# Performance work log

Hardware: AMD Instinct MI355X
Metric: run time of the kernel (lower is better)

## Reference

```python
import jax, jax.numpy as jnp
import numpy as np


def setup_inputs() -> dict:
    key = jax.random.key(0)
    k1, k2, k3 = jax.random.split(key, 3)
    N, D_IN, D_OUT = 8192, 512, 256
    x = jax.random.normal(k1, (N, D_IN), dtype=jnp.float32)
    # binary dense adjacency (nonzero pattern is what the torch loop uses)
    adj = jax.random.randint(k2, (N, N), 0, 2, dtype=jnp.int32)
    # weight init in torch is uniform(-stdv, stdv), stdv = 1/sqrt(out_features);
    # a normal init is fine for a numerical reference
    W = jax.random.normal(k3, (D_IN, D_OUT), dtype=jnp.float32) * (1.0 / np.sqrt(D_OUT))
    return {"x": x, "adj": adj, "W": W}


def reference(x, adj, W):
    # output = X @ W  (multiply_add(self.weight, input, None) -> mm(input, weight))
    xw = jnp.matmul(x, W)  # [N, D_OUT]
    # per-node unweighted mean over neighbors given by nonzero(adj[i])
    a = (adj != 0).astype(xw.dtype)          # [N, N] binary
    deg = jnp.sum(a, axis=1, keepdims=True)  # [N, 1] neighbor counts
    out = jnp.matmul(a, xw) / deg            # D^{-1} A (X W)
    return out
```

## Files before the change

kernel.cpp:

```cpp
#include <hip/hip_runtime.h>
#include <stdint.h>

typedef __attribute__((ext_vector_type(8))) short  bf16x8;
typedef __attribute__((ext_vector_type(4))) float  f32x4;
typedef __attribute__((ext_vector_type(4))) int    int4v;
typedef __attribute__((ext_vector_type(4))) float  float4v;
typedef __attribute__((ext_vector_type(4))) unsigned int uint4v;
typedef __attribute__((ext_vector_type(2))) unsigned int uint2v;

#define NN   8192
#define DIN  512
#define DOUT 256
#define NW   (NN / 32)

#define BM2     256
#define KSPLIT2 8
#define KS2     (NN / KSPLIT2)
#define BK2     64
#define NTK     (KS2 / BK2)

#define MFMA16(a, b, c) __builtin_amdgcn_mfma_f32_16x16x32_bf16((a), (b), (c), 0, 0, 0)

__device__ __forceinline__ unsigned short f2bf(float f) {
  unsigned u = __float_as_uint(f);
  return (unsigned short)((u + 0x7FFFu + ((u >> 16) & 1u)) >> 16);
}

__device__ __forceinline__ void gld16(const void* g, void* s) {
  __builtin_amdgcn_global_load_lds(
      (const __attribute__((address_space(1))) unsigned int*)g,
      (__attribute__((address_space(3))) unsigned int*)s, 16, 0, 0);
}

__global__ void k_wt(const float* __restrict__ W, unsigned short* __restrict__ Wt) {
  int n = blockIdx.x;
  for (int c = threadIdx.x; c < DIN; c += blockDim.x)
    Wt[n * DIN + c] = f2bf(W[c * DOUT + n]);
}

__global__ __launch_bounds__(256) void k_xwt(const float* __restrict__ x,
                                             const unsigned short* __restrict__ Wt,
                                             unsigned short* __restrict__ xw_t) {
  const int mb = blockIdx.x >> 1, nb = blockIdx.x & 1;
  const int tid = threadIdx.x;
  const int w = tid >> 6, l = tid & 63;
  const int wm = w >> 1, wn = w & 1;
  const int lr = l & 15, lg = l >> 4;
  const int m_base = mb * 128 + wm * 64;
  const int n_base = nb * 128 + wn * 64;

  f32x4 acc[4][4];
  for (int i = 0; i < 4; ++i)
    for (int j = 0; j < 4; ++j) acc[i][j] = (f32x4)0.0f;

  for (int c0 = 0; c0 < DIN; c0 += 32) {
    const int c = c0 + lg * 8;
    bf16x8 af[4], bfv[4];
#pragma unroll
    for (int mt = 0; mt < 4; ++mt) {
      const float* xp = x + (size_t)(m_base + mt * 16 + lr) * DIN + c;
      float4v x0 = *reinterpret_cast<const float4v*>(xp);
      float4v x1 = *reinterpret_cast<const float4v*>(xp + 4);
      bf16x8 a;
#pragma unroll
      for (int j = 0; j < 4; ++j) {
        a[j]     = (short)f2bf(x0[j]);
        a[4 + j] = (short)f2bf(x1[j]);
      }
      af[mt] = a;
    }
#pragma unroll
    for (int nt = 0; nt < 4; ++nt)
      bfv[nt] = *reinterpret_cast<const bf16x8*>(Wt + (size_t)(n_base + nt * 16 + lr) * DIN + c);
#pragma unroll
    for (int mt = 0; mt < 4; ++mt)
#pragma unroll
      for (int nt = 0; nt < 4; ++nt)
        acc[mt][nt] = MFMA16(af[mt], bfv[nt], acc[mt][nt]);
  }

#pragma unroll
  for (int nt = 0; nt < 4; ++nt) {
    const int n = n_base + nt * 16 + lr;
#pragma unroll
    for (int mt = 0; mt < 4; ++mt) {
      const int m = m_base + mt * 16 + lg * 4;
      unsigned short b0 = f2bf(acc[mt][nt][0]), b1 = f2bf(acc[mt][nt][1]);
      unsigned short b2 = f2bf(acc[mt][nt][2]), b3 = f2bf(acc[mt][nt][3]);
      uint2v p;
      p[0] = (unsigned)b0 | ((unsigned)b1 << 16);
      p[1] = (unsigned)b2 | ((unsigned)b3 << 16);
      *reinterpret_cast<uint2v*>(xw_t + (size_t)n * NN + m) = p;
    }
  }
}

__global__ __launch_bounds__(256) void k_pack(const int* __restrict__ adj,
                                              unsigned int* __restrict__ bits,
                                              int* __restrict__ deg) {
  __shared__ int wsum[4];
  const int tid = threadIdx.x;
  const int w = tid >> 6, l = tid & 63;
  const int row = blockIdx.x;
  const int* src = adj + (size_t)row * NN + w * 2048 + l;
  unsigned long long* bdst =
      reinterpret_cast<unsigned long long*>(bits + (size_t)row * NW + w * 64);

  int cnt = 0;
#pragma unroll
  for (int it = 0; it < 32; it += 8) {
    unsigned long long b[8];
#pragma unroll
    for (int u = 0; u < 8; ++u)
      b[u] = __ballot(src[(it + u) * 64] != 0);
#pragma unroll
    for (int u = 0; u < 8; ++u) {
      if (l == 0) bdst[it + u] = b[u];
      cnt += (int)__popcll(b[u]);
    }
  }

  if (l == 0) wsum[w] = cnt;
  __syncthreads();
  if (tid == 0) deg[row] = wsum[0] + wsum[1] + wsum[2] + wsum[3];
}

__global__ __launch_bounds__(512, 2) void k_agg(const unsigned int* __restrict__ bits,
                                                const unsigned short* __restrict__ xw_t,
                                                float* __restrict__ outp) {
  __shared__ unsigned short Bs[2][16384];

  const int tid = threadIdx.x;
  const int w = tid >> 6, l = tid & 63;
  const int lr = l & 15, lg = l >> 4;
  const int wm = w >> 2, wn = w & 3;

  const int bid = blockIdx.x;
  const int ks = bid & 7;
  const int rb = bid >> 3;
  const int row0 = rb * BM2;

  const int sn = tid >> 3;
  const int sj = tid & 7;
  const unsigned short* gB = xw_t + (size_t)sn * NN + ks * KS2 + ((sj ^ (sn & 7)) * 8);

  const unsigned int* gA = bits + (size_t)(row0 + wm * 128 + lr) * NW + ks * (KS2 >> 5);

  f32x4 acc[8][4];
#pragma unroll
  for (int i = 0; i < 8; ++i)
#pragma unroll
    for (int j = 0; j < 4; ++j) acc[i][j] = (f32x4)0.0f;

  uint2v Ab[8], An[8];

#define STAGE_B(t, buf) do {                                                   \
    _Pragma("unroll")                                                          \
    for (int p_ = 0; p_ < 4; ++p_)                                             \
      gld16(gB + (size_t)p_ * 64 * NN + (t) * BK2,                             \
            (char*)&Bs[buf][0] + p_ * 8192 + w * 1024);                        \
  } while (0)

#define LOADA(t, arr) do {                                                     \
    _Pragma("unroll")                                                          \
    for (int mf_ = 0; mf_ < 8; ++mf_)                                          \
      arr[mf_] = *reinterpret_cast<const uint2v*>(gA + (size_t)mf_ * 16 * NW + 2 * (t)); \
  } while (0)

#define COMPUTE(buf) do {                                                      \
    _Pragma("unroll")                                                          \
    for (int kf_ = 0; kf_ < 2; ++kf_) {                                        \
      bf16x8 bf_[4];                                                           \
      _Pragma("unroll")                                                        \
      for (int nf_ = 0; nf_ < 4; ++nf_) {                                      \
        const int n_ = wn * 64 + nf_ * 16 + lr;                                \
        bf_[nf_] = *reinterpret_cast<const bf16x8*>(                           \
            &Bs[buf][n_ * 64 + (((kf_ * 4 + lg) ^ (n_ & 7)) * 8)]);            \
      }                                                                        \
      _Pragma("unroll")                                                        \
      for (int mf_ = 0; mf_ < 8; ++mf_) {                                      \
        const unsigned a32_ = Ab[mf_][kf_];                                    \
        uint4v q_;                                                             \
        _Pragma("unroll")                                                      \
        for (int j_ = 0; j_ < 4; ++j_) {                                       \
          unsigned b2_ = (a32_ >> (lg * 8 + 2 * j_)) & 3u;                     \
          q_[j_] = ((b2_ | (b2_ << 15)) & 0x10001u) * 0x3F80u;                 \
        }                                                                      \
        const bf16x8 af_ = *reinterpret_cast<const bf16x8*>(&q_);              \
        acc[mf_][0] = MFMA16(af_, bf_[0], acc[mf_][0]);                        \
        acc[mf_][1] = MFMA16(af_, bf_[1], acc[mf_][1]);                        \
        acc[mf_][2] = MFMA16(af_, bf_[2], acc[mf_][2]);                        \
        acc[mf_][3] = MFMA16(af_, bf_[3], acc[mf_][3]);                        \
      }                                                                        \
    }                                                                          \
  } while (0)

  STAGE_B(0, 0);
  LOADA(0, Ab);
  __syncthreads();

  for (int t = 0; t < NTK; ++t) {
    const int buf = t & 1;
    if (t + 1 < NTK) {
      STAGE_B(t + 1, buf ^ 1);
      LOADA(t + 1, An);
    }
    COMPUTE(buf);
#pragma unroll
    for (int mf = 0; mf < 8; ++mf) Ab[mf] = An[mf];
    __syncthreads();
  }
#undef STAGE_B
#undef LOADA
#undef COMPUTE

  float* po = outp + (size_t)ks * NN * DOUT;
#pragma unroll
  for (int mf = 0; mf < 8; ++mf)
#pragma unroll
    for (int nf = 0; nf < 4; ++nf)
#pragma unroll
      for (int r = 0; r < 4; ++r) {
        const int row = row0 + wm * 128 + mf * 16 + lg * 4 + r;
        const int col = wn * 64 + nf * 16 + lr;
        po[(size_t)row * DOUT + col] = acc[mf][nf][r];
      }
}

__global__ __launch_bounds__(256) void k_div(const float* __restrict__ outp,
                                             const int* __restrict__ deg,
                                             float* __restrict__ out) {
  const int idx = blockIdx.x * 256 + threadIdx.x;
  const size_t i4 = (size_t)idx * 4;
  const int row = (int)(i4 >> 8);
  float4v s = *reinterpret_cast<const float4v*>(outp + i4);
#pragma unroll
  for (int p = 1; p < KSPLIT2; ++p) {
    float4v v = *reinterpret_cast<const float4v*>(outp + (size_t)p * NN * DOUT + i4);
    s[0] += v[0]; s[1] += v[1]; s[2] += v[2]; s[3] += v[3];
  }
  const float sc = 1.0f / (float)deg[row];
  s[0] *= sc; s[1] *= sc; s[2] *= sc; s[3] *= sc;
  *reinterpret_cast<float4v*>(out + i4) = s;
}

extern "C" void kernel_launch(void* const* d_in, const int* in_sizes, int n_in,
                              void* d_out, int out_size, void* d_ws, size_t ws_size,
                              hipStream_t stream) {
  const float* x   = (const float*)d_in[0];
  const int*   adj = (const int*)d_in[1];
  const float* W   = (const float*)d_in[2];
  float* out = (float*)d_out;

  char* ws = (char*)d_ws;
  unsigned short* xw_t = (unsigned short*)ws;
  unsigned short* Wt   = (unsigned short*)(ws + (size_t)4 * 1024 * 1024);
  int*            deg  = (int*)(ws + (size_t)4 * 1024 * 1024 + 512 * 1024);
  unsigned int*   bits = (unsigned int*)(ws + (size_t)5 * 1024 * 1024);
  float*          outp = (float*)(ws + (size_t)16 * 1024 * 1024);

  k_wt<<<256, 128, 0, stream>>>(W, Wt);
  k_xwt<<<128, 256, 0, stream>>>(x, Wt, xw_t);
  k_pack<<<NN, 256, 0, stream>>>(adj, bits, deg);
  k_agg<<<(NN / BM2) * KSPLIT2, 512, 0, stream>>>(bits, xw_t, outp);
  k_div<<<(NN * DOUT) / (256 * 4), 256, 0, stream>>>(outp, deg, out);
}
```

Baseline: 152.1 us.

## Fuse adjacency packing into aggregation GEMM, reading int32 adj directly

Removes the separate bit-packing kernel and has the aggregation kernel load raw int32 adjacency tiles, convert them to bf16 0/1 values in LDS, and accumulate per-split degree counts. The degree is then summed across splits in the final divide kernel. This saves one kernel launch and the write and read of the bitmask, but each aggregation block now streams the full 256MB int32 adjacency (each element read once) and spends extra LDS space and conversion ALU inside the main loop.

After: 180.2 us. 1.19x slower.

```diff
diff --git a/kernel.cpp b/kernel.cpp
--- a/kernel.cpp
+++ b/kernel.cpp
@@ -11,7 +11,6 @@
 #define NN   8192
 #define DIN  512
 #define DOUT 256
-#define NW   (NN / 32)
 
 #define BM2     256
 #define KSPLIT2 8
@@ -20,6 +19,7 @@
 #define NTK     (KS2 / BK2)
 
 #define MFMA16(a, b, c) __builtin_amdgcn_mfma_f32_16x16x32_bf16((a), (b), (c), 0, 0, 0)
+#define PK2(a, b) (((0u - (unsigned)(a)) & 0x3F80u) | (((0u - (unsigned)(b)) & 0x3F80u) << 16))
 
 __device__ __forceinline__ unsigned short f2bf(float f) {
   unsigned u = __float_as_uint(f);
@@ -95,39 +95,11 @@
   }
 }
 
-__global__ __launch_bounds__(256) void k_pack(const int* __restrict__ adj,
-                                              unsigned int* __restrict__ bits,
-                                              int* __restrict__ deg) {
-  __shared__ int wsum[4];
-  const int tid = threadIdx.x;
-  const int w = tid >> 6, l = tid & 63;
-  const int row = blockIdx.x;
-  const int* src = adj + (size_t)row * NN + w * 2048 + l;
-  unsigned long long* bdst =
-      reinterpret_cast<unsigned long long*>(bits + (size_t)row * NW + w * 64);
-
-  int cnt = 0;
-#pragma unroll
-  for (int it = 0; it < 32; it += 8) {
-    unsigned long long b[8];
-#pragma unroll
-    for (int u = 0; u < 8; ++u)
-      b[u] = __ballot(src[(it + u) * 64] != 0);
-#pragma unroll
-    for (int u = 0; u < 8; ++u) {
-      if (l == 0) bdst[it + u] = b[u];
-      cnt += (int)__popcll(b[u]);
-    }
-  }
-
-  if (l == 0) wsum[w] = cnt;
-  __syncthreads();
-  if (tid == 0) deg[row] = wsum[0] + wsum[1] + wsum[2] + wsum[3];
-}
-
-__global__ __launch_bounds__(512, 2) void k_agg(const unsigned int* __restrict__ bits,
+__global__ __launch_bounds__(512, 2) void k_agg(const int* __restrict__ adj,
                                                 const unsigned short* __restrict__ xw_t,
-                                                float* __restrict__ outp) {
+                                                float* __restrict__ outp,
+                                                int* __restrict__ degp) {
+  __shared__ unsigned short Abf[2][BM2 * 64];
   __shared__ unsigned short Bs[2][16384];
 
   const int tid = threadIdx.x;
@@ -139,12 +111,15 @@
   const int ks = bid & 7;
   const int rb = bid >> 3;
   const int row0 = rb * BM2;
+  const int kbase = ks * KS2;
+
+  const int sr = tid >> 1;
+  const int c2 = tid & 1;
+  const int* gApt = adj + (size_t)(row0 + sr) * NN + kbase + c2 * 32;
 
   const int sn = tid >> 3;
   const int sj = tid & 7;
-  const unsigned short* gB = xw_t + (size_t)sn * NN + ks * KS2 + ((sj ^ (sn & 7)) * 8);
-
-  const unsigned int* gA = bits + (size_t)(row0 + wm * 128 + lr) * NW + ks * (KS2 >> 5);
+  const unsigned short* gB = xw_t + (size_t)sn * NN + kbase + ((sj ^ (sn & 7)) * 8);
 
   f32x4 acc[8][4];
 #pragma unroll
@@ -152,7 +127,14 @@
 #pragma unroll
     for (int j = 0; j < 4; ++j) acc[i][j] = (f32x4)0.0f;
 
-  uint2v Ab[8], An[8];
+  int4v ar[8];
+  int cnt = 0;
+
+#define LOAD_RAWA(t) do {                                                      \
+    _Pragma("unroll")                                                          \
+    for (int i_ = 0; i_ < 8; ++i_)                                             \
+      ar[i_] = *reinterpret_cast<const int4v*>(gApt + (size_t)(t) * BK2 + i_ * 4); \
+  } while (0)
 
 #define STAGE_B(t, buf) do {                                                   \
     _Pragma("unroll")                                                          \
@@ -161,10 +143,21 @@
             (char*)&Bs[buf][0] + p_ * 8192 + w * 1024);                        \
   } while (0)
 
-#define LOADA(t, arr) do {                                                     \
-    _Pragma("unroll")                                                          \
-    for (int mf_ = 0; mf_ < 8; ++mf_)                                          \
-      arr[mf_] = *reinterpret_cast<const uint2v*>(gA + (size_t)mf_ * 16 * NW + 2 * (t)); \
+#define CVT_WRITE_A(buf) do {                                                  \
+    _Pragma("unroll")                                                          \
+    for (int i_ = 0; i_ < 8; ++i_)                                             \
+      cnt += ar[i_][0] + ar[i_][1] + ar[i_][2] + ar[i_][3];                    \
+    _Pragma("unroll")                                                          \
+    for (int q_ = 0; q_ < 4; ++q_) {                                           \
+      uint4v dq_;                                                              \
+      _Pragma("unroll")                                                        \
+      for (int j_ = 0; j_ < 4; ++j_) {                                         \
+        const int d_ = q_ * 4 + j_;                                            \
+        dq_[j_] = PK2(ar[d_ >> 1][(d_ & 1) * 2], ar[d_ >> 1][(d_ & 1) * 2 + 1]); \
+      }                                                                        \
+      const int bsw_ = ((c2 * 4 + q_) ^ (sr & 7)) * 8;                         \
+      *reinterpret_cast<uint4v*>(&Abf[buf][sr * 64 + bsw_]) = dq_;             \
+    }                                                                          \
   } while (0)
 
 #define COMPUTE(buf) do {                                                      \
@@ -179,14 +172,9 @@
       }                                                                        \
       _Pragma("unroll")                                                        \
       for (int mf_ = 0; mf_ < 8; ++mf_) {                                      \
-        const unsigned a32_ = Ab[mf_][kf_];                                    \
-        uint4v q_;                                                             \
-        _Pragma("unroll")                                                      \
-        for (int j_ = 0; j_ < 4; ++j_) {                                       \
-          unsigned b2_ = (a32_ >> (lg * 8 + 2 * j_)) & 3u;                     \
-          q_[j_] = ((b2_ | (b2_ << 15)) & 0x10001u) * 0x3F80u;                 \
-        }                                                                      \
-        const bf16x8 af_ = *reinterpret_cast<const bf16x8*>(&q_);              \
+        const int r_ = wm * 128 + mf_ * 16 + lr;                               \
+        const bf16x8 af_ = *reinterpret_cast<const bf16x8*>(                   \
+            &Abf[buf][r_ * 64 + (((kf_ * 4 + lg) ^ (r_ & 7)) * 8)]);           \
         acc[mf_][0] = MFMA16(af_, bf_[0], acc[mf_][0]);                        \
         acc[mf_][1] = MFMA16(af_, bf_[1], acc[mf_][1]);                        \
         acc[mf_][2] = MFMA16(af_, bf_[2], acc[mf_][2]);                        \
@@ -195,24 +183,28 @@
     }                                                                          \
   } while (0)
 
+  LOAD_RAWA(0);
   STAGE_B(0, 0);
-  LOADA(0, Ab);
+  CVT_WRITE_A(0);
   __syncthreads();
 
   for (int t = 0; t < NTK; ++t) {
     const int buf = t & 1;
     if (t + 1 < NTK) {
+      LOAD_RAWA(t + 1);
       STAGE_B(t + 1, buf ^ 1);
-      LOADA(t + 1, An);
     }
     COMPUTE(buf);
-#pragma unroll
-    for (int mf = 0; mf < 8; ++mf) Ab[mf] = An[mf];
+    if (t + 1 < NTK) CVT_WRITE_A(buf ^ 1);
     __syncthreads();
   }
+#undef LOAD_RAWA
 #undef STAGE_B
-#undef LOADA
+#undef CVT_WRITE_A
 #undef COMPUTE
+
+  cnt += __shfl_xor(cnt, 1);
+  if (c2 == 0) degp[ks * NN + row0 + sr] = cnt;
 
   float* po = outp + (size_t)ks * NN * DOUT;
 #pragma unroll
@@ -228,7 +220,7 @@
 }
 
 __global__ __launch_bounds__(256) void k_div(const float* __restrict__ outp,
-                                             const int* __restrict__ deg,
+                                             const int* __restrict__ degp,
                                              float* __restrict__ out) {
   const int idx = blockIdx.x * 256 + threadIdx.x;
   const size_t i4 = (size_t)idx * 4;
@@ -239,7 +231,10 @@
     float4v v = *reinterpret_cast<const float4v*>(outp + (size_t)p * NN * DOUT + i4);
     s[0] += v[0]; s[1] += v[1]; s[2] += v[2]; s[3] += v[3];
   }
-  const float sc = 1.0f / (float)deg[row];
+  int d = 0;
+#pragma unroll
+  for (int p = 0; p < KSPLIT2; ++p) d += degp[p * NN + row];
+  const float sc = 1.0f / (float)d;
   s[0] *= sc; s[1] *= sc; s[2] *= sc; s[3] *= sc;
   *reinterpret_cast<float4v*>(out + i4) = s;
 }
@@ -255,13 +250,11 @@
   char* ws = (char*)d_ws;
   unsigned short* xw_t = (unsigned short*)ws;
   unsigned short* Wt   = (unsigned short*)(ws + (size_t)4 * 1024 * 1024);
-  int*            deg  = (int*)(ws + (size_t)4 * 1024 * 1024 + 512 * 1024);
-  unsigned int*   bits = (unsigned int*)(ws + (size_t)5 * 1024 * 1024);
+  int*            degp = (int*)(ws + (size_t)4 * 1024 * 1024 + 512 * 1024);
   float*          outp = (float*)(ws + (size_t)16 * 1024 * 1024);
 
   k_wt<<<256, 128, 0, stream>>>(W, Wt);
   k_xwt<<<128, 256, 0, stream>>>(x, Wt, xw_t);
-  k_pack<<<NN, 256, 0, stream>>>(adj, bits, deg);
-  k_agg<<<(NN / BM2) * KSPLIT2, 512, 0, stream>>>(bits, xw_t, outp);
-  k_div<<<(NN * DOUT) / (256 * 4), 256, 0, stream>>>(outp, deg, out);
-}
+  k_agg<<<(NN / BM2) * KSPLIT2, 512, 0, stream>>>(adj, xw_t, outp, degp);
+  k_div<<<(NN * DOUT) / (256 * 4), 256, 0, stream>>>(outp, degp, out);
+}
```
